# Performance work log

Hardware: AMD Instinct MI355X
Metric: run time of the kernel (lower is better)

## Reference

```python
import jax, jax.numpy as jnp
import numpy as np
import math

B, L, E, H = 512, 200, 64, 4
D = E // H
NEG = jnp.float32(-(2.0 ** 32) + 1.0)


def setup_inputs() -> dict:
    key = jax.random.key(0)
    ks = jax.random.split(key, 12)
    inp = jax.random.normal(ks[0], (B, L, E), dtype=jnp.float32)
    # realistic variable-length histories: mask[b, t] = t < len_b, len_b in [1, L]
    lens = jax.random.randint(ks[1], (B, 1), 1, L + 1)
    mask = jnp.arange(L)[None, :] < lens  # [B, L] bool
    s = 1.0 / math.sqrt(E)
    pos_enc = jax.random.normal(ks[2], (1, L, E), dtype=jnp.float32)
    Wk = jax.random.uniform(ks[3], (E, E), jnp.float32, -s, s)
    bk = jnp.zeros((E,), jnp.float32)
    Wv = jax.random.uniform(ks[4], (E, E), jnp.float32, -s, s)
    bv = jnp.zeros((E,), jnp.float32)
    Wq = jax.random.uniform(ks[5], (E, E), jnp.float32, -s, s)
    bq = jnp.zeros((E,), jnp.float32)
    Wf = jax.random.uniform(ks[6], (E, E), jnp.float32, -s, s)
    bf = jnp.zeros((E,), jnp.float32)
    return {"input": inp, "mask": mask, "pos_enc": pos_enc,
            "Wk": Wk, "bk": bk, "Wv": Wv, "bv": bv,
            "Wq": Wq, "bq": bq, "Wf": Wf, "bf": bf}


def reference(input, mask, pos_enc, Wk, bk, Wv, bv, Wq, bq, Wf, bf):
    x = input + pos_enc  # [B, L, E]
    # project and split heads: [B, H, L, D]
    def split(t):
        return t.reshape(B, L, H, D).transpose(0, 2, 1, 3)
    k = split(x @ Wk.T + bk)
    v = split(x @ Wv.T + bv)
    q = split(x @ Wq.T + bq) / math.sqrt(D)
    scores = jnp.einsum('bhqd,bhkd->bhqk', q, k)  # [B, H, L, L]
    # key_mask in torch code broadcasts over dim 3 (mask on the QUERY axis),
    # query_mask is its transpose (mask on the KEY axis). Combined: both must be valid.
    both = mask[:, None, :, None] & mask[:, None, None, :]  # [B, 1, L, L]
    scores = jnp.where(both, scores, NEG)
    attn = jax.nn.softmax(scores, axis=-1)
    # dropout is identity at inference; omitted deterministically
    out = jnp.einsum('bhqk,bhkd->bhqd', attn, v)
    out = out.transpose(0, 2, 1, 3).reshape(B, L, E)
    out = out @ Wf.T + bf
    fm = mask.astype(jnp.float32)[:, :, None]  # [B, L, 1]
    lens = jnp.sum(fm, axis=1)  # [B, 1]
    pooled = jnp.sum(out * fm, axis=1) / (lens + 1e-8)  # [B, E]
    return pooled
```

## Files before the change

kernel.cpp:

```cpp
#include <hip/hip_runtime.h>
#include <hip/hip_fp16.h>
#include <math.h>

#define Bn 512
#define Ln 200
#define En 64
#define Hn 4
#define Dn 16
#define NT13 13
#define RMAX 208
#define XS 72
#define KS 36
#define VS 212
#define QSC 0.36067376022224085f

typedef _Float16 __f16;
typedef __f16 f16x4 __attribute__((ext_vector_type(4)));
typedef __f16 f16x8 __attribute__((ext_vector_type(8)));
typedef float f32x4 __attribute__((ext_vector_type(4)));

#if __has_builtin(__builtin_amdgcn_exp2f)
__device__ __forceinline__ float fexp2(float x) { return __builtin_amdgcn_exp2f(x); }
#else
__device__ __forceinline__ float fexp2(float x) { return exp2f(x); }
#endif

__device__ __forceinline__ f16x8 pack8(float4 a, float4 b) {
    f16x8 r;
    r[0] = (__f16)a.x; r[1] = (__f16)a.y; r[2] = (__f16)a.z; r[3] = (__f16)a.w;
    r[4] = (__f16)b.x; r[5] = (__f16)b.y; r[6] = (__f16)b.z; r[7] = (__f16)b.w;
    return r;
}

__global__ __launch_bounds__(256, 3) void fused_kernel(
    const float* __restrict__ input, const int* __restrict__ mask,
    const float* __restrict__ pos_enc,
    const float* __restrict__ Wk, const float* __restrict__ bk,
    const float* __restrict__ Wv, const float* __restrict__ bv,
    const float* __restrict__ Wq, const float* __restrict__ bq,
    const float* __restrict__ Wf, const float* __restrict__ bf_,
    float* __restrict__ out)
{
    __shared__ __align__(16) __f16 xw[4][16 * XS];
    __shared__ __align__(16) __f16 Kh[RMAX * KS];
    __shared__ __align__(16) __f16 Qh[RMAX * KS];
    __shared__ __align__(16) __f16 Vt[32 * VS];
    __shared__ float red[4][16];
    __shared__ float ph[32];
    __shared__ int cnt_red[4];

    const int tid  = threadIdx.x;
    const int b    = blockIdx.x >> 1, hp = blockIdx.x & 1;
    const int wave = tid >> 6, lane = tid & 63;
    const int quad = lane >> 4, ln16 = lane & 15;

    int c = 0;
    for (int t = tid; t < Ln; t += 256) c += (mask[b * Ln + t] != 0) ? 1 : 0;

    f16x8 bfr[3][2][2];
    #pragma unroll
    for (int m = 0; m < 3; ++m) {
        const float* W = (m == 0) ? Wk : (m == 1) ? Wv : Wq;
        #pragma unroll
        for (int ct = 0; ct < 2; ++ct)
            #pragma unroll
            for (int ks = 0; ks < 2; ++ks) {
                const float4* wp = (const float4*)(W + (size_t)(hp * 32 + ct * 16 + ln16) * 64) + (ks * 8 + quad * 2);
                bfr[m][ct][ks] = pack8(wp[0], wp[1]);
            }
    }
    float bkv[2], bvv[2], bqv[2];
    #pragma unroll
    for (int ct = 0; ct < 2; ++ct) {
        int cg = hp * 32 + ct * 16 + ln16;
        bkv[ct] = bk[cg]; bvv[ct] = bv[cg]; bqv[ct] = bq[cg];
    }

    const float4* in4 = (const float4*)(input + (size_t)b * Ln * En);
    const float4* pe4 = (const float4*)pos_enc;
    __f16* myx = xw[wave];

    for (int rt = wave; rt < NT13; rt += 4) {
        #pragma unroll
        for (int i = 0; i < 4; ++i) {
            const int gi = lane + (i << 6);
            const int r = gi >> 4, c4 = gi & 15;
            const int R = rt * 16 + r;
            float4 xv = {0,0,0,0}, pv = {0,0,0,0};
            if (R < Ln) { xv = in4[R * 16 + c4]; pv = pe4[R * 16 + c4]; }
            f16x4 hx;
            hx[0] = (__f16)(xv.x + pv.x); hx[1] = (__f16)(xv.y + pv.y);
            hx[2] = (__f16)(xv.z + pv.z); hx[3] = (__f16)(xv.w + pv.w);
            *(f16x4*)(myx + r * XS + c4 * 4) = hx;
        }

        f16x8 af[2];
        #pragma unroll
        for (int ks = 0; ks < 2; ++ks)
            af[ks] = *(const f16x8*)(myx + ln16 * XS + ks * 32 + quad * 8);

        f32x4 acc[3][2];
        #pragma unroll
        for (int m = 0; m < 3; ++m)
            #pragma unroll
            for (int ct = 0; ct < 2; ++ct) acc[m][ct] = (f32x4){0,0,0,0};
        #pragma unroll
        for (int ks = 0; ks < 2; ++ks)
            #pragma unroll
            for (int m = 0; m < 3; ++m)
                #pragma unroll
                for (int ct = 0; ct < 2; ++ct)
                    acc[m][ct] = __builtin_amdgcn_mfma_f32_16x16x32_f16(af[ks], bfr[m][ct][ks], acc[m][ct], 0, 0, 0);

        #pragma unroll
        for (int ct = 0; ct < 2; ++ct) {
            #pragma unroll
            for (int j = 0; j < 4; ++j) {
                int t = rt * 16 + quad * 4 + j;
                Kh[t * KS + ct * 16 + ln16] = (__f16)(acc[0][ct][j] + bkv[ct]);
                Qh[t * KS + ct * 16 + ln16] = (__f16)((acc[2][ct][j] + bqv[ct]) * QSC);
            }
            f16x4 vp;
            #pragma unroll
            for (int j = 0; j < 4; ++j) vp[j] = (__f16)(acc[1][ct][j] + bvv[ct]);
            *(f16x4*)(Vt + (ct * 16 + ln16) * VS + rt * 16 + quad * 4) = vp;
        }
    }

    #pragma unroll
    for (int off = 32; off; off >>= 1) c += __shfl_down(c, off, 64);
    if (lane == 0) cnt_red[wave] = c;
    __syncthreads();
    const int len = cnt_red[0] + cnt_red[1] + cnt_red[2] + cnt_red[3];
    const int nt = (len + 15) >> 4;

    const int hl = wave >> 1;
    const int hoff = hl * 16;
    const int nquad = (nt + 3) >> 2;
    f32x4 pool = {0.f, 0.f, 0.f, 0.f};

    for (int g = (wave & 1); g < nquad; g += 2) {
        const int qt0 = 4 * g;
        f16x4 qf[4];
        #pragma unroll
        for (int i = 0; i < 4; ++i) {
            int qr = min((qt0 + i) * 16 + ln16, RMAX - 1);
            qf[i] = *(const f16x4*)(Qh + qr * KS + hoff + quad * 4);
        }
        f32x4 o2[4];
        float l[4] = {0.f, 0.f, 0.f, 0.f};
        #pragma unroll
        for (int i = 0; i < 4; ++i) o2[i] = (f32x4){0,0,0,0};

        f16x4 kf = *(const f16x4*)(Kh + ln16 * KS + hoff + quad * 4);
        f16x4 vf = *(const f16x4*)(Vt + (hoff + ln16) * VS + quad * 4);

        for (int kt = 0; kt < nt - 1; ++kt) {
            const f16x4 kfn = *(const f16x4*)(Kh + ((kt + 1) * 16 + ln16) * KS + hoff + quad * 4);
            const f16x4 vfn = *(const f16x4*)(Vt + (hoff + ln16) * VS + (kt + 1) * 16 + quad * 4);
            f32x4 s[4];
            #pragma unroll
            for (int i = 0; i < 4; ++i)
                s[i] = __builtin_amdgcn_mfma_f32_16x16x16f16(kf, qf[i], (f32x4){0,0,0,0}, 0, 0, 0);
            f16x4 pf[4];
            #pragma unroll
            for (int i = 0; i < 4; ++i) {
                #pragma unroll
                for (int j = 0; j < 4; ++j) {
                    float p = fexp2(fminf(s[i][j], 14.5f));
                    l[i] += p;
                    pf[i][j] = (__f16)p;
                }
            }
            #pragma unroll
            for (int i = 0; i < 4; ++i)
                o2[i] = __builtin_amdgcn_mfma_f32_16x16x16f16(vf, pf[i], o2[i], 0, 0, 0);
            kf = kfn; vf = vfn;
        }
        {
            const int kbase = (nt - 1) * 16 + quad * 4;
            f32x4 s[4];
            #pragma unroll
            for (int i = 0; i < 4; ++i)
                s[i] = __builtin_amdgcn_mfma_f32_16x16x16f16(kf, qf[i], (f32x4){0,0,0,0}, 0, 0, 0);
            f16x4 pf[4];
            #pragma unroll
            for (int i = 0; i < 4; ++i) {
                #pragma unroll
                for (int j = 0; j < 4; ++j) {
                    const bool kok = (kbase + j) < len;
                    float p = kok ? fexp2(fminf(s[i][j], 14.5f)) : 0.f;
                    l[i] += p;
                    pf[i][j] = (__f16)p;
                }
            }
            #pragma unroll
            for (int i = 0; i < 4; ++i)
                o2[i] = __builtin_amdgcn_mfma_f32_16x16x16f16(vf, pf[i], o2[i], 0, 0, 0);
        }

        #pragma unroll
        for (int i = 0; i < 4; ++i) {
            l[i] += __shfl_xor(l[i], 16, 64);
            l[i] += __shfl_xor(l[i], 32, 64);
            const float rs = ((qt0 + i) * 16 + ln16 < len) ? 1.f / l[i] : 0.f;
            #pragma unroll
            for (int j = 0; j < 4; ++j) pool[j] = fmaf(o2[i][j], rs, pool[j]);
        }
    }

    #pragma unroll
    for (int j = 0; j < 4; ++j) {
        #pragma unroll
        for (int off = 1; off < 16; off <<= 1) pool[j] += __shfl_xor(pool[j], off, 64);
    }
    if (ln16 == 0) {
        #pragma unroll
        for (int j = 0; j < 4; ++j) red[wave][quad * 4 + j] = pool[j];
    }
    __syncthreads();
    if (tid < 32) {
        int hl2 = tid >> 4, vd = tid & 15;
        float sres = red[hl2 * 2][vd] + red[hl2 * 2 + 1][vd];
        ph[tid] = sres / ((float)len + 1e-8f);
    }
    __syncthreads();

    if (tid < 64) {
        const int e = tid;
        const float* wr = Wf + (size_t)e * 64 + hp * 32;
        float a = (hp == 0) ? bf_[e] : 0.f;
        #pragma unroll
        for (int i = 0; i < 32; ++i) a = fmaf(wr[i], ph[i], a);
        atomicAdd(out + b * En + e, a);
    }
}

extern "C" void kernel_launch(void* const* d_in, const int* in_sizes, int n_in,
                              void* d_out, int out_size, void* d_ws, size_t ws_size,
                              hipStream_t stream) {
    const float* input   = (const float*)d_in[0];
    const int*   mask    = (const int*)  d_in[1];
    const float* pos_enc = (const float*)d_in[2];
    const float* Wk      = (const float*)d_in[3];
    const float* bk      = (const float*)d_in[4];
    const float* Wv      = (const float*)d_in[5];
    const float* bv      = (const float*)d_in[6];
    const float* Wq      = (const float*)d_in[7];
    const float* bq      = (const float*)d_in[8];
    const float* Wf      = (const float*)d_in[9];
    const float* bf      = (const float*)d_in[10];

    float* out = (float*)d_out;
    hipMemsetAsync(out, 0, (size_t)Bn * En * sizeof(float), stream);

    fused_kernel<<<Bn * 2, 256, 0, stream>>>(input, mask, pos_enc,
                                             Wk, bk, Wv, bv, Wq, bq, Wf, bf, out);
}
```

Baseline: 125.8 us.

## Drop X staging buffer, shrink LDS arrays, raise occupancy to four blocks

Removes the per-wave LDS staging of input+pos_enc and loads the MFMA A-fragments straight from global memory, adding pos_enc while packing to fp16. The K/Q/V LDS arrays shrink to exactly Ln rows with tighter strides, with bounds guards on the writes and clamped reads in the attention loop. Launch bounds go from three to four blocks per CU to exploit the smaller LDS footprint. Risks include extra register pressure under the tighter launch bound and LDS bank conflicts from the new strides (QS2=32 has no padding).

```diff
diff --git a/kernel.cpp b/kernel.cpp
--- a/kernel.cpp
+++ b/kernel.cpp
@@ -8,10 +8,9 @@
 #define Hn 4
 #define Dn 16
 #define NT13 13
-#define RMAX 208
-#define XS 72
-#define KS 36
-#define VS 212
+#define KS2 34
+#define QS2 32
+#define VS2 200
 #define QSC 0.36067376022224085f
 
 typedef _Float16 __f16;
@@ -25,6 +24,14 @@
 __device__ __forceinline__ float fexp2(float x) { return exp2f(x); }
 #endif
 
+__device__ __forceinline__ f16x8 pack8s(float4 a, float4 b, float4 pa, float4 pb) {
+    f16x8 r;
+    r[0] = (__f16)(a.x + pa.x); r[1] = (__f16)(a.y + pa.y);
+    r[2] = (__f16)(a.z + pa.z); r[3] = (__f16)(a.w + pa.w);
+    r[4] = (__f16)(b.x + pb.x); r[5] = (__f16)(b.y + pb.y);
+    r[6] = (__f16)(b.z + pb.z); r[7] = (__f16)(b.w + pb.w);
+    return r;
+}
 __device__ __forceinline__ f16x8 pack8(float4 a, float4 b) {
     f16x8 r;
     r[0] = (__f16)a.x; r[1] = (__f16)a.y; r[2] = (__f16)a.z; r[3] = (__f16)a.w;
@@ -32,7 +39,7 @@
     return r;
 }
 
-__global__ __launch_bounds__(256, 3) void fused_kernel(
+__global__ __launch_bounds__(256, 4) void fused_kernel(
     const float* __restrict__ input, const int* __restrict__ mask,
     const float* __restrict__ pos_enc,
     const float* __restrict__ Wk, const float* __restrict__ bk,
@@ -41,10 +48,9 @@
     const float* __restrict__ Wf, const float* __restrict__ bf_,
     float* __restrict__ out)
 {
-    __shared__ __align__(16) __f16 xw[4][16 * XS];
-    __shared__ __align__(16) __f16 Kh[RMAX * KS];
-    __shared__ __align__(16) __f16 Qh[RMAX * KS];
-    __shared__ __align__(16) __f16 Vt[32 * VS];
+    __shared__ __align__(16) __f16 Kh[Ln * KS2];
+    __shared__ __align__(16) __f16 Qh[Ln * QS2];
+    __shared__ __align__(16) __f16 Vt[32 * VS2];
     __shared__ float red[4][16];
     __shared__ float ph[32];
     __shared__ int cnt_red[4];
@@ -78,26 +84,22 @@
 
     const float4* in4 = (const float4*)(input + (size_t)b * Ln * En);
     const float4* pe4 = (const float4*)pos_enc;
-    __f16* myx = xw[wave];
 
     for (int rt = wave; rt < NT13; rt += 4) {
-        #pragma unroll
-        for (int i = 0; i < 4; ++i) {
-            const int gi = lane + (i << 6);
-            const int r = gi >> 4, c4 = gi & 15;
-            const int R = rt * 16 + r;
-            float4 xv = {0,0,0,0}, pv = {0,0,0,0};
-            if (R < Ln) { xv = in4[R * 16 + c4]; pv = pe4[R * 16 + c4]; }
-            f16x4 hx;
-            hx[0] = (__f16)(xv.x + pv.x); hx[1] = (__f16)(xv.y + pv.y);
-            hx[2] = (__f16)(xv.z + pv.z); hx[3] = (__f16)(xv.w + pv.w);
-            *(f16x4*)(myx + r * XS + c4 * 4) = hx;
-        }
-
+        const int R = rt * 16 + ln16;
+        const bool rok = (R < Ln);
         f16x8 af[2];
         #pragma unroll
-        for (int ks = 0; ks < 2; ++ks)
-            af[ks] = *(const f16x8*)(myx + ln16 * XS + ks * 32 + quad * 8);
+        for (int ks = 0; ks < 2; ++ks) {
+            float4 xa = {0,0,0,0}, xb = {0,0,0,0}, pa = {0,0,0,0}, pb = {0,0,0,0};
+            if (rok) {
+                const int o4 = R * 16 + ks * 8 + quad * 2;
+                xa = in4[o4]; xb = in4[o4 + 1];
+                pa = pe4[o4 - R * 16 + (R % Ln) * 16];
+                pb = pe4[o4 - R * 16 + (R % Ln) * 16 + 1];
+            }
+            af[ks] = pack8s(xa, xb, pa, pb);
+        }
 
         f32x4 acc[3][2];
         #pragma unroll
@@ -116,14 +118,19 @@
         for (int ct = 0; ct < 2; ++ct) {
             #pragma unroll
             for (int j = 0; j < 4; ++j) {
-                int t = rt * 16 + quad * 4 + j;
-                Kh[t * KS + ct * 16 + ln16] = (__f16)(acc[0][ct][j] + bkv[ct]);
-                Qh[t * KS + ct * 16 + ln16] = (__f16)((acc[2][ct][j] + bqv[ct]) * QSC);
-            }
-            f16x4 vp;
-            #pragma unroll
-            for (int j = 0; j < 4; ++j) vp[j] = (__f16)(acc[1][ct][j] + bvv[ct]);
-            *(f16x4*)(Vt + (ct * 16 + ln16) * VS + rt * 16 + quad * 4) = vp;
+                const int t = rt * 16 + quad * 4 + j;
+                if (t < Ln) {
+                    Kh[t * KS2 + ct * 16 + ln16] = (__f16)(acc[0][ct][j] + bkv[ct]);
+                    Qh[t * QS2 + ct * 16 + ln16] = (__f16)((acc[2][ct][j] + bqv[ct]) * QSC);
+                }
+            }
+            const int vc0 = rt * 16 + quad * 4;
+            if (vc0 < Ln) {
+                f16x4 vp;
+                #pragma unroll
+                for (int j = 0; j < 4; ++j) vp[j] = (__f16)(acc[1][ct][j] + bvv[ct]);
+                *(f16x4*)(Vt + (ct * 16 + ln16) * VS2 + vc0) = vp;
+            }
         }
     }
 
@@ -144,20 +151,22 @@
         f16x4 qf[4];
         #pragma unroll
         for (int i = 0; i < 4; ++i) {
-            int qr = min((qt0 + i) * 16 + ln16, RMAX - 1);
-            qf[i] = *(const f16x4*)(Qh + qr * KS + hoff + quad * 4);
+            int qr = min((qt0 + i) * 16 + ln16, Ln - 1);
+            qf[i] = *(const f16x4*)(Qh + qr * QS2 + hoff + quad * 4);
         }
         f32x4 o2[4];
         float l[4] = {0.f, 0.f, 0.f, 0.f};
         #pragma unroll
         for (int i = 0; i < 4; ++i) o2[i] = (f32x4){0,0,0,0};
 
-        f16x4 kf = *(const f16x4*)(Kh + ln16 * KS + hoff + quad * 4);
-        f16x4 vf = *(const f16x4*)(Vt + (hoff + ln16) * VS + quad * 4);
+        f16x4 kf = *(const f16x4*)(Kh + ln16 * KS2 + hoff + quad * 4);
+        f16x4 vf = *(const f16x4*)(Vt + (hoff + ln16) * VS2 + quad * 4);
 
         for (int kt = 0; kt < nt - 1; ++kt) {
-            const f16x4 kfn = *(const f16x4*)(Kh + ((kt + 1) * 16 + ln16) * KS + hoff + quad * 4);
-            const f16x4 vfn = *(const f16x4*)(Vt + (hoff + ln16) * VS + (kt + 1) * 16 + quad * 4);
+            const int krn = min((kt + 1) * 16 + ln16, Ln - 1);
+            const int vcn = min((kt + 1) * 16 + quad * 4, Ln - 4);
+            const f16x4 kfn = *(const f16x4*)(Kh + krn * KS2 + hoff + quad * 4);
+            const f16x4 vfn = *(const f16x4*)(Vt + (hoff + ln16) * VS2 + vcn);
             f32x4 s[4];
             #pragma unroll
             for (int i = 0; i < 4; ++i)
```

Result: no change. 123.7 us (-1.7%).
